# Performance work log

Hardware: AMD Instinct MI355X
Metric: run time of the kernel (lower is better)

## Reference

```python
import jax, jax.numpy as jnp
import numpy as np

D_MODEL = 1024
N_HEADS = 16
D_K = D_MODEL // N_HEADS
LN_EPS = 1e-5


def setup_inputs() -> dict:
    key = jax.random.key(0)
    ks = jax.random.split(key, 10)
    s = 1.0 / np.sqrt(D_MODEL)
    x = jax.random.normal(ks[0], (8, 1024, D_MODEL), dtype=jnp.float32)
    return {
        "x": x,
        "Wq": jax.random.uniform(ks[1], (D_MODEL, D_MODEL), jnp.float32, -s, s),
        "bq": jax.random.uniform(ks[2], (D_MODEL,), jnp.float32, -s, s),
        "Wk": jax.random.uniform(ks[3], (D_MODEL, D_MODEL), jnp.float32, -s, s),
        "bk": jax.random.uniform(ks[4], (D_MODEL,), jnp.float32, -s, s),
        "Wv": jax.random.uniform(ks[5], (D_MODEL, D_MODEL), jnp.float32, -s, s),
        "bv": jax.random.uniform(ks[6], (D_MODEL,), jnp.float32, -s, s),
        "Wo": jax.random.uniform(ks[7], (D_MODEL, D_MODEL), jnp.float32, -s, s),
        "bo": jax.random.uniform(ks[8], (D_MODEL,), jnp.float32, -s, s),
        "gamma": jnp.ones((D_MODEL,), jnp.float32),
        "beta": jnp.zeros((D_MODEL,), jnp.float32),
    }


def reference(x, Wq, bq, Wk, bk, Wv, bv, Wo, bo, gamma, beta):
    B, S, D = x.shape
    H, dk = N_HEADS, D_K
    # projections -> [B, H, S, dk]
    q = (x @ Wq.T + bq).reshape(B, S, H, dk).transpose(0, 2, 1, 3)
    k = (x @ Wk.T + bk).reshape(B, S, H, dk).transpose(0, 2, 1, 3)
    v = (x @ Wv.T + bv).reshape(B, S, H, dk).transpose(0, 2, 1, 3)
    scores = jnp.einsum('bhqd,bhkd->bhqk', q, k) / jnp.sqrt(jnp.float32(dk))
    attn = jax.nn.softmax(scores, axis=-1)  # dropout: eval mode (identity)
    ctx = jnp.einsum('bhqk,bhkd->bhqd', attn, v)
    ctx = ctx.transpose(0, 2, 1, 3).reshape(B, S, D)
    out = ctx @ Wo.T + bo
    h = out + x  # residual
    mu = jnp.mean(h, axis=-1, keepdims=True)
    var = jnp.mean((h - mu) ** 2, axis=-1, keepdims=True)
    y = (h - mu) * jax.lax.rsqrt(var + LN_EPS) * gamma + beta
    return y, attn
```

## Files before the change

### kernel.cpp

```cpp
#include <hip/hip_runtime.h>
#include <math.h>

#define D 1024
#define H 16
#define DK 64
#define SQ 1024
#define NB 8
#define NROW (NB*SQ)

typedef __attribute__((ext_vector_type(8))) short bf16x8;
typedef __attribute__((ext_vector_type(4))) float f32x4;

__device__ __forceinline__ ushort f2bf(float x){
    unsigned u = __builtin_bit_cast(unsigned, x);
    u += 0x7FFFu + ((u >> 16) & 1u);
    return (ushort)(u >> 16);
}
__device__ __forceinline__ float bf2f(ushort u){
    return __builtin_bit_cast(float, (unsigned)u << 16);
}

__device__ __forceinline__ f32x4 mfma16(bf16x8 a, bf16x8 b, f32x4 c){
    return __builtin_amdgcn_mfma_f32_16x16x32_bf16(a, b, c, 0, 0, 0);
}

__device__ __forceinline__ void gload16(const void* g, void* l){
    __builtin_amdgcn_global_load_lds(
        (const __attribute__((address_space(1))) unsigned int*)g,
        (__attribute__((address_space(3))) unsigned int*)l, 16, 0, 0);
}

__device__ __forceinline__ bf16x8 gld8(const ushort* p){
    return __builtin_bit_cast(bf16x8, *(const uint4*)p);
}

__global__ __launch_bounds__(256)
void cvt_all(const float* __restrict__ x,
             const float* __restrict__ Wq, const float* __restrict__ Wk,
             const float* __restrict__ Wv, const float* __restrict__ Wo,
             ushort* __restrict__ xb, ushort* __restrict__ wb_)
{
    const int bid = blockIdx.x;
    const float* s; ushort* d; size_t off;
    if (bid < 4096) { s = x; d = xb; off = (size_t)bid * 2048; }
    else {
        int r = bid - 4096;
        int wsel = r >> 9;
        if      (wsel == 0) s = Wq;
        else if (wsel == 1) s = Wk;
        else if (wsel == 2) s = Wv;
        else                s = Wo;
        d = wb_ + (size_t)wsel * 1048576;
        off = (size_t)(r & 511) * 2048;
    }
    size_t i = off + (size_t)threadIdx.x * 8;
    float4 a = *(const float4*)(s + i);
    float4 b = *(const float4*)(s + i + 4);
    ushort tmp[8] = {f2bf(a.x),f2bf(a.y),f2bf(a.z),f2bf(a.w),
                     f2bf(b.x),f2bf(b.y),f2bf(b.z),f2bf(b.w)};
    *(uint4*)(d + i) = *(uint4*)tmp;
}

__device__ __forceinline__ void stage_g(const ushort* __restrict__ g, int ldg,
                                        ushort* lds, int t)
{
#pragma unroll
    for (int i = 0; i < 2; ++i){
        int c = i*256 + t;
        int row = c >> 2, sc = c & 3;
        int gch = sc ^ (row & 3);
        gload16(g + (size_t)row*ldg + gch*8, lds + c*8);
    }
}
__device__ __forceinline__ bf16x8 gfrag(const ushort* lds, int row, int kc)
{
    uint4 v = ((const uint4*)lds)[row*4 + (kc ^ (row & 3))];
    return __builtin_bit_cast(bf16x8, v);
}

__global__ __launch_bounds__(256)
void gemm_qkv(const ushort* __restrict__ A, const ushort* __restrict__ Wp,
              const float* __restrict__ bq, const float* __restrict__ bk,
              const float* __restrict__ bv,
              ushort* __restrict__ Qb, ushort* __restrict__ Kb,
              ushort* __restrict__ Vtb)
{
    __shared__ ushort As[4096];
    __shared__ ushort Bs[4096];
    const int t = threadIdx.x, lane = t & 63, w = t >> 6;
    const int wr = w >> 1, wc = w & 1, lr = lane & 15, kg = lane >> 4;
    const int bx = blockIdx.x % 24, by = blockIdx.x / 24;
    const int i0 = by * 128, j0 = bx * 128;
    const int section = bx >> 3;
    const ushort* Ab = A  + (size_t)i0 * 1024;
    const ushort* Wb = Wp + (size_t)j0 * 1024;
    const float* bias = (section == 0) ? bq : (section == 1) ? bk : bv;
    ushort* outp      = (section == 0) ? Qb : (section == 1) ? Kb : Vtb;

    f32x4 acc[4][4];
#pragma unroll
    for (int m = 0; m < 4; ++m)
#pragma unroll
        for (int n = 0; n < 4; ++n) acc[m][n] = (f32x4){0.f,0.f,0.f,0.f};

    for (int k0 = 0; k0 < 1024; k0 += 32){
        __syncthreads();
        stage_g(Ab + k0, 1024, As, t);
        stage_g(Wb + k0, 1024, Bs, t);
        __syncthreads();
        bf16x8 af[4], bfr[4];
#pragma unroll
        for (int m = 0; m < 4; ++m) af[m]  = gfrag(As, wr*64 + m*16 + lr, kg);
#pragma unroll
        for (int n = 0; n < 4; ++n) bfr[n] = gfrag(Bs, wc*64 + n*16 + lr, kg);
#pragma unroll
        for (int m = 0; m < 4; ++m)
#pragma unroll
            for (int n = 0; n < 4; ++n)
                acc[m][n] = mfma16(af[m], bfr[n], acc[m][n]);
    }

#pragma unroll
    for (int m = 0; m < 4; ++m){
        int rt = i0 + wr*64 + m*16 + kg*4;
#pragma unroll
        for (int n = 0; n < 4; ++n){
            int jc = ((j0 + wc*64 + n*16 + lr) & 1023);
            float bj = bias[jc];
            int hh = jc >> 6, dd = jc & 63;
#pragma unroll
            for (int j = 0; j < 4; ++j){
                int i = rt + j;
                int b = i >> 10, s = i & 1023;
                float v = acc[m][n][j] + bj;
                size_t idx = (section < 2)
                    ? ((((size_t)b*H + hh)*SQ + s)*DK + dd)
                    : ((((size_t)b*H + hh)*DK + dd)*SQ + s);
                outp[idx] = f2bf(v);
            }
        }
    }
}

__global__ __launch_bounds__(256)
void gemm_o(const ushort* __restrict__ A, const ushort* __restrict__ W,
            const float* __restrict__ bias, const float* __restrict__ resid,
            float* __restrict__ out)
{
    __shared__ ushort As[4096];
    __shared__ ushort Bs[4096];
    const int t = threadIdx.x, lane = t & 63, w = t >> 6;
    const int wr = w >> 1, wc = w & 1, lr = lane & 15, kg = lane >> 4;
    const int i0 = blockIdx.y * 128, j0 = blockIdx.x * 128;
    const ushort* Ab = A + (size_t)i0 * 1024;
    const ushort* Wb = W + (size_t)j0 * 1024;

    f32x4 acc[4][4];
#pragma unroll
    for (int m = 0; m < 4; ++m)
#pragma unroll
        for (int n = 0; n < 4; ++n) acc[m][n] = (f32x4){0.f,0.f,0.f,0.f};

    for (int k0 = 0; k0 < 1024; k0 += 32){
        __syncthreads();
        stage_g(Ab + k0, 1024, As, t);
        stage_g(Wb + k0, 1024, Bs, t);
        __syncthreads();
        bf16x8 af[4], bfr[4];
#pragma unroll
        for (int m = 0; m < 4; ++m) af[m]  = gfrag(As, wr*64 + m*16 + lr, kg);
#pragma unroll
        for (int n = 0; n < 4; ++n) bfr[n] = gfrag(Bs, wc*64 + n*16 + lr, kg);
#pragma unroll
        for (int m = 0; m < 4; ++m)
#pragma unroll
            for (int n = 0; n < 4; ++n)
                acc[m][n] = mfma16(af[m], bfr[n], acc[m][n]);
    }

#pragma unroll
    for (int m = 0; m < 4; ++m){
        int rt = i0 + wr*64 + m*16 + kg*4;
#pragma unroll
        for (int n = 0; n < 4; ++n){
            int ct = j0 + wc*64 + n*16 + lr;
            float bj = bias[ct];
#pragma unroll
            for (int j = 0; j < 4; ++j){
                int i = rt + j;
                out[(size_t)i*1024 + ct] = acc[m][n][j] + bj + resid[(size_t)i*1024 + ct];
            }
        }
    }
}

__device__ __forceinline__ void stage64x64(const ushort* __restrict__ g, int ldg,
                                           ushort* lds, int t)
{
#pragma unroll
    for (int i = 0; i < 2; ++i){
        int c = i*256 + t;
        int row = c >> 3, sc = c & 7;
        int gch = sc ^ (row & 7);
        gload16(g + (size_t)row*ldg + gch*8, lds + c*8);
    }
}
__device__ __forceinline__ bf16x8 frag_ld(const ushort* lds, int row, int chunk)
{
    uint4 v = ((const uint4*)lds)[row*8 + (chunk ^ (row & 7))];
    return __builtin_bit_cast(bf16x8, v);
}

__global__ __launch_bounds__(256)
void attn_v6(const ushort* __restrict__ Q, const ushort* __restrict__ K,
             const ushort* __restrict__ Vt, float* __restrict__ attn_out,
             ushort* __restrict__ ctx)
{
    __shared__ ushort KV[2][8192];
    __shared__ ushort Ps[4][1024];

    const int t    = threadIdx.x;
    const int lane = t & 63;
    const int w    = t >> 6;
    const int lr   = lane & 15, kg = lane >> 4;
    const int bid  = blockIdx.x;
    const int qt   = bid >> 7, bh = bid & 127;
    const int b    = bh >> 4, hh = bh & 15;
    const size_t base = (size_t)bh * SQ * DK;

    bf16x8 qf[2];
    {
        const ushort* qrow = Q + base + (size_t)(qt*64 + w*16 + lr) * DK + kg*8;
        qf[0] = gld8(qrow);
        qf[1] = gld8(qrow + 32);
    }

    const float CEXP = 0.18033688011112042f;

    float lsum[4] = {0.f, 0.f, 0.f, 0.f};
    stage64x64(K + base, DK, KV[0], t);
    for (int kt = 0; kt < 16; ++kt) {
        const int cur = kt & 1;
        __syncthreads();
        if (kt < 15)
            stage64x64(K + base + (size_t)(kt+1)*64*DK, DK, KV[cur^1], t);
        const ushort* Ks = KV[cur];
#pragma unroll
        for (int n = 0; n < 4; ++n) {
            f32x4 z = {0.f,0.f,0.f,0.f};
            z = mfma16(qf[0], frag_ld(Ks, n*16+lr, kg),   z);
            z = mfma16(qf[1], frag_ld(Ks, n*16+lr, 4+kg), z);
#pragma unroll
            for (int r = 0; r < 4; ++r)
                lsum[r] += exp2f(z[r] * CEXP);
        }
    }
    float invl[4];
#pragma unroll
    for (int r = 0; r < 4; ++r) {
        float s = lsum[r];
#pragma unroll
        for (int msk = 1; msk < 16; msk <<= 1) s += __shfl_xor(s, msk, 64);
        invl[r] = 1.0f / s;
    }

    f32x4 acc_o[4];
#pragma unroll
    for (int n = 0; n < 4; ++n) acc_o[n] = (f32x4){0.f,0.f,0.f,0.f};

    float* ap0 = attn_out + ((size_t)bh*SQ + (size_t)qt*64 + w*16)*SQ;
    ushort* pw = &Ps[w][0];

    stage64x64(K  + base, DK, KV[0],        t);
    stage64x64(Vt + base, SQ, KV[0] + 4096, t);

    for (int kt = 0; kt < 16; ++kt) {
        const int cur = kt & 1;
        __syncthreads();
        if (kt < 15) {
            stage64x64(K  + base + (size_t)(kt+1)*64*DK, DK, KV[cur^1],        t);
            stage64x64(Vt + base + (size_t)(kt+1)*64,    SQ, KV[cur^1] + 4096, t);
        }
        const ushort* Ks = KV[cur];
        const ushort* Vs = KV[cur] + 4096;

        f32x4 sc[4];
#pragma unroll
        for (int n = 0; n < 4; ++n) {
            f32x4 z = {0.f,0.f,0.f,0.f};
            z = mfma16(qf[0], frag_ld(Ks, n*16+lr, kg),   z);
            z = mfma16(qf[1], frag_ld(Ks, n*16+lr, 4+kg), z);
            sc[n] = z;
        }
#pragma unroll
        for (int n = 0; n < 4; ++n) {
#pragma unroll
            for (int r = 0; r < 4; ++r) {
                float p = exp2f(sc[n][r] * CEXP) * invl[r];
                int row = kg*4 + r, col = n*16 + lr;
                pw[row*64 + ((col>>3) ^ (row&7))*8 + (col&7)] = f2bf(p);
            }
        }
        bf16x8 a0 = frag_ld(pw, lr, kg);
        bf16x8 a1 = frag_ld(pw, lr, 4+kg);
#pragma unroll
        for (int n = 0; n < 4; ++n) {
            acc_o[n] = mfma16(a0, frag_ld(Vs, n*16+lr, kg),   acc_o[n]);
            acc_o[n] = mfma16(a1, frag_ld(Vs, n*16+lr, 4+kg), acc_o[n]);
        }
#pragma unroll
        for (int rr = 0; rr < 4; ++rr) {
            int row = kg*4 + rr;
            int cidx = row*64 + ((lr>>1) ^ (row&7))*8 + (lr&1)*4;
            uint2 pk = *(const uint2*)(pw + cidx);
            float4 o;
            o.x = bf2f((ushort)(pk.x & 0xFFFF));
            o.y = bf2f((ushort)(pk.x >> 16));
            o.z = bf2f((ushort)(pk.y & 0xFFFF));
            o.w = bf2f((ushort)(pk.y >> 16));
            *(float4*)(ap0 + (size_t)row*SQ + kt*64 + lr*4) = o;
        }
    }

    ushort* cp = ctx + ((size_t)b*SQ + (size_t)qt*64 + w*16)*D + hh*DK;
#pragma unroll
    for (int n = 0; n < 4; ++n)
#pragma unroll
        for (int r = 0; r < 4; ++r)
            cp[(size_t)(kg*4+r)*D + n*16 + lr] = f2bf(acc_o[n][r]);
}

__global__ __launch_bounds__(256)
void ln_k(const float* __restrict__ hbuf, const float* __restrict__ gamma,
          const float* __restrict__ beta, float* __restrict__ y)
{
    const int row = blockIdx.x, t = threadIdx.x;
    float4 v = ((const float4*)(hbuf + (size_t)row * D))[t];
    float s  = v.x + v.y + v.z + v.w;
    float sq = v.x*v.x + v.y*v.y + v.z*v.z + v.w*v.w;
#pragma unroll
    for (int o = 32; o >= 1; o >>= 1) {
        s  += __shfl_down(s, o, 64);
        sq += __shfl_down(sq, o, 64);
    }
    __shared__ float rs_[4], rq_[4], mu_s, rstd_s;
    int wid = t >> 6;
    if ((t & 63) == 0) { rs_[wid] = s; rq_[wid] = sq; }
    __syncthreads();
    if (t == 0) {
        float S  = rs_[0]+rs_[1]+rs_[2]+rs_[3];
        float Q2 = rq_[0]+rq_[1]+rq_[2]+rq_[3];
        float mu  = S * (1.0f/1024.0f);
        float var = Q2 * (1.0f/1024.0f) - mu*mu;
        mu_s = mu; rstd_s = rsqrtf(var + 1e-5f);
    }
    __syncthreads();
    float mu = mu_s, rstd = rstd_s;
    float4 g = ((const float4*)gamma)[t];
    float4 be = ((const float4*)beta)[t];
    float4 o;
    o.x = (v.x-mu)*rstd*g.x + be.x;
    o.y = (v.y-mu)*rstd*g.y + be.y;
    o.z = (v.z-mu)*rstd*g.z + be.z;
    o.w = (v.w-mu)*rstd*g.w + be.w;
    ((float4*)(y + (size_t)row * D))[t] = o;
}

extern "C" void kernel_launch(void* const* d_in, const int* in_sizes, int n_in,
                              void* d_out, int out_size, void* d_ws, size_t ws_size,
                              hipStream_t stream)
{
    const float* x     = (const float*)d_in[0];
    const float* Wq    = (const float*)d_in[1];
    const float* bq    = (const float*)d_in[2];
    const float* Wk    = (const float*)d_in[3];
    const float* bk    = (const float*)d_in[4];
    const float* Wv    = (const float*)d_in[5];
    const float* bv    = (const float*)d_in[6];
    const float* Wo    = (const float*)d_in[7];
    const float* bo    = (const float*)d_in[8];
    const float* gamma = (const float*)d_in[9];
    const float* beta  = (const float*)d_in[10];

    float* y    = (float*)d_out;
    float* attn = (float*)d_out + (size_t)NROW * D;

    const size_t SZ  = (size_t)NROW * D;
    const size_t WSZ = (size_t)D * D;
    ushort* ws   = (ushort*)d_ws;
    ushort* xb   = ws;
    ushort* Wpk  = xb  + SZ;
    ushort* Wob  = Wpk + 3*WSZ;
    ushort* Qb   = Wob + WSZ;
    ushort* Kb   = Qb  + SZ;
    ushort* Vtb  = Kb  + SZ;
    ushort* Cb   = Vtb + SZ;
    float*  Hb   = (float*)(Cb + SZ);

    cvt_all<<<6144, 256, 0, stream>>>(x, Wq, Wk, Wv, Wo, xb, Wpk);

    gemm_qkv<<<1536, 256, 0, stream>>>(xb, Wpk, bq, bk, bv, Qb, Kb, Vtb);

    attn_v6<<<2048, 256, 0, stream>>>(Qb, Kb, Vtb, attn, Cb);

    gemm_o<<<dim3(8, 64), 256, 0, stream>>>(Cb, Wob, bo, x, Hb);

    ln_k<<<NROW, 256, 0, stream>>>(Hb, gamma, beta, y);
}
```

Measured before the change: 336.2 us.

## Process 128 query rows per attention block with 512 threads and MFMA priority

The attention kernel now launches half as many blocks, each with 8 waves covering 128 query rows instead of 64, so every staged K/V tile in LDS serves twice as many queries. The staging helper is rewritten so each of the 512 threads loads one 16-byte chunk. The per-wave P scratch buffer grows to 8 slots. s_setprio calls raise wave priority around the MFMA sections so matrix work is favoured over other waves' memory work. The larger block may lower occupancy and scheduling flexibility on a kernel that is largely bound by writing the attention matrix.

```diff
diff --git a/kernel.cpp b/kernel.cpp
--- a/kernel.cpp
+++ b/kernel.cpp
@@ -194,16 +194,12 @@
     }
 }
 
-__device__ __forceinline__ void stage64x64(const ushort* __restrict__ g, int ldg,
-                                           ushort* lds, int t)
-{
-#pragma unroll
-    for (int i = 0; i < 2; ++i){
-        int c = i*256 + t;
-        int row = c >> 3, sc = c & 7;
-        int gch = sc ^ (row & 7);
-        gload16(g + (size_t)row*ldg + gch*8, lds + c*8);
-    }
+__device__ __forceinline__ void stage64x64_512(const ushort* __restrict__ g, int ldg,
+                                               ushort* lds, int t)
+{
+    int row = t >> 3, sc = t & 7;
+    int gch = sc ^ (row & 7);
+    gload16(g + (size_t)row*ldg + gch*8, lds + t*8);
 }
 __device__ __forceinline__ bf16x8 frag_ld(const ushort* lds, int row, int chunk)
 {
@@ -211,13 +207,13 @@
     return __builtin_bit_cast(bf16x8, v);
 }
 
-__global__ __launch_bounds__(256)
-void attn_v6(const ushort* __restrict__ Q, const ushort* __restrict__ K,
+__global__ __launch_bounds__(512)
+void attn_v8(const ushort* __restrict__ Q, const ushort* __restrict__ K,
              const ushort* __restrict__ Vt, float* __restrict__ attn_out,
              ushort* __restrict__ ctx)
 {
     __shared__ ushort KV[2][8192];
-    __shared__ ushort Ps[4][1024];
+    __shared__ ushort Ps[8][1024];
 
     const int t    = threadIdx.x;
     const int lane = t & 63;
@@ -230,7 +226,7 @@
 
     bf16x8 qf[2];
     {
-        const ushort* qrow = Q + base + (size_t)(qt*64 + w*16 + lr) * DK + kg*8;
+        const ushort* qrow = Q + base + (size_t)(qt*128 + w*16 + lr) * DK + kg*8;
         qf[0] = gld8(qrow);
         qf[1] = gld8(qrow + 32);
     }
@@ -238,13 +234,14 @@
     const float CEXP = 0.18033688011112042f;
 
     float lsum[4] = {0.f, 0.f, 0.f, 0.f};
-    stage64x64(K + base, DK, KV[0], t);
+    stage64x64_512(K + base, DK, KV[0], t);
     for (int kt = 0; kt < 16; ++kt) {
         const int cur = kt & 1;
         __syncthreads();
         if (kt < 15)
-            stage64x64(K + base + (size_t)(kt+1)*64*DK, DK, KV[cur^1], t);
+            stage64x64_512(K + base + (size_t)(kt+1)*64*DK, DK, KV[cur^1], t);
         const ushort* Ks = KV[cur];
+        __builtin_amdgcn_s_setprio(1);
 #pragma unroll
         for (int n = 0; n < 4; ++n) {
             f32x4 z = {0.f,0.f,0.f,0.f};
@@ -254,6 +251,7 @@
             for (int r = 0; r < 4; ++r)
                 lsum[r] += exp2f(z[r] * CEXP);
         }
+        __builtin_amdgcn_s_setprio(0);
     }
     float invl[4];
 #pragma unroll
@@ -268,23 +266,24 @@
 #pragma unroll
     for (int n = 0; n < 4; ++n) acc_o[n] = (f32x4){0.f,0.f,0.f,0.f};
 
-    float* ap0 = attn_out + ((size_t)bh*SQ + (size_t)qt*64 + w*16)*SQ;
+    float* ap0 = attn_out + ((size_t)bh*SQ + (size_t)qt*128 + w*16)*SQ;
     ushort* pw = &Ps[w][0];
 
-    stage64x64(K  + base, DK, KV[0],        t);
-    stage64x64(Vt + base, SQ, KV[0] + 4096, t);
+    stage64x64_512(K  + base, DK, KV[0],        t);
+    stage64x64_512(Vt + base, SQ, KV[0] + 4096, t);
 
     for (int kt = 0; kt < 16; ++kt) {
         const int cur = kt & 1;
         __syncthreads();
         if (kt < 15) {
-            stage64x64(K  + base + (size_t)(kt+1)*64*DK, DK, KV[cur^1],        t);
-            stage64x64(Vt + base + (size_t)(kt+1)*64,    SQ, KV[cur^1] + 4096, t);
+            stage64x64_512(K  + base + (size_t)(kt+1)*64*DK, DK, KV[cur^1],        t);
+            stage64x64_512(Vt + base + (size_t)(kt+1)*64,    SQ, KV[cur^1] + 4096, t);
         }
         const ushort* Ks = KV[cur];
         const ushort* Vs = KV[cur] + 4096;
 
         f32x4 sc[4];
+        __builtin_amdgcn_s_setprio(1);
 #pragma unroll
         for (int n = 0; n < 4; ++n) {
             f32x4 z = {0.f,0.f,0.f,0.f};
@@ -292,6 +291,7 @@
             z = mfma16(qf[1], frag_ld(Ks, n*16+lr, 4+kg), z);
             sc[n] = z;
         }
+        __builtin_amdgcn_s_setprio(0);
 #pragma unroll
         for (int n = 0; n < 4; ++n) {
 #pragma unroll
@@ -303,11 +303,13 @@
         }
         bf16x8 a0 = frag_ld(pw, lr, kg);
         bf16x8 a1 = frag_ld(pw, lr, 4+kg);
+        __builtin_amdgcn_s_setprio(1);
 #pragma unroll
         for (int n = 0; n < 4; ++n) {
             acc_o[n] = mfma16(a0, frag_ld(Vs, n*16+lr, kg),   acc_o[n]);
             acc_o[n] = mfma16(a1, frag_ld(Vs, n*16+lr, 4+kg), acc_o[n]);
         }
+        __builtin_amdgcn_s_setprio(0);
 #pragma unroll
         for (int rr = 0; rr < 4; ++rr) {
             int row = kg*4 + rr;
@@ -322,7 +324,7 @@
         }
     }
 
-    ushort* cp = ctx + ((size_t)b*SQ + (size_t)qt*64 + w*16)*D + hh*DK;
+    ushort* cp = ctx + ((size_t)b*SQ + (size_t)qt*128 + w*16)*D + hh*DK;
 #pragma unroll
     for (int n = 0; n < 4; ++n)
 #pragma unroll
@@ -401,7 +403,7 @@
 
     gemm_qkv<<<1536, 256, 0, stream>>>(xb, Wpk, bq, bk, bv, Qb, Kb, Vtb);
 
-    attn_v6<<<2048, 256, 0, stream>>>(Qb, Kb, Vtb, attn, Cb);
+    attn_v8<<<1024, 512, 0, stream>>>(Qb, Kb, Vtb, attn, Cb);
 
     gemm_o<<<dim3(8, 64), 256, 0, stream>>>(Cb, Wob, bo, x, Hb);
 
```

After: 349.0 us. 1.04x slower.

## Split attention into unnormalized ctx pass and separate attn-matrix write kernel

Applied to the files above, without the earlier changes.

The fused attention kernel used to run two passes over K: one for row sums and one for probabilities, ctx and the attn matrix. It now computes ctx from unnormalized exponentials, accumulates the row sums in the same loop, scales ctx at the end and saves the inverse sums to a buffer. A new second kernel recomputes QK^T and writes the normalized fp32 attn matrix. This takes V loads and the bf16 round-trip out of the attn-write path but adds a kernel launch. The attn values are no longer bf16-rounded, and the written attn is in a strided per-lane pattern rather than float4 stores.

```diff
diff --git a/kernel.cpp b/kernel.cpp
--- a/kernel.cpp
+++ b/kernel.cpp
@@ -15,9 +15,6 @@
     unsigned u = __builtin_bit_cast(unsigned, x);
     u += 0x7FFFu + ((u >> 16) & 1u);
     return (ushort)(u >> 16);
-}
-__device__ __forceinline__ float bf2f(ushort u){
-    return __builtin_bit_cast(float, (unsigned)u << 16);
 }
 
 __device__ __forceinline__ f32x4 mfma16(bf16x8 a, bf16x8 b, f32x4 c){
@@ -212,9 +209,9 @@
 }
 
 __global__ __launch_bounds__(256)
-void attn_v6(const ushort* __restrict__ Q, const ushort* __restrict__ K,
-             const ushort* __restrict__ Vt, float* __restrict__ attn_out,
-             ushort* __restrict__ ctx)
+void attn_ctx(const ushort* __restrict__ Q, const ushort* __restrict__ K,
+              const ushort* __restrict__ Vt, float* __restrict__ invb,
+              ushort* __restrict__ ctx)
 {
     __shared__ ushort KV[2][8192];
     __shared__ ushort Ps[4][1024];
@@ -238,37 +235,10 @@
     const float CEXP = 0.18033688011112042f;
 
     float lsum[4] = {0.f, 0.f, 0.f, 0.f};
-    stage64x64(K + base, DK, KV[0], t);
-    for (int kt = 0; kt < 16; ++kt) {
-        const int cur = kt & 1;
-        __syncthreads();
-        if (kt < 15)
-            stage64x64(K + base + (size_t)(kt+1)*64*DK, DK, KV[cur^1], t);
-        const ushort* Ks = KV[cur];
-#pragma unroll
-        for (int n = 0; n < 4; ++n) {
-            f32x4 z = {0.f,0.f,0.f,0.f};
-            z = mfma16(qf[0], frag_ld(Ks, n*16+lr, kg),   z);
-            z = mfma16(qf[1], frag_ld(Ks, n*16+lr, 4+kg), z);
-#pragma unroll
-            for (int r = 0; r < 4; ++r)
-                lsum[r] += exp2f(z[r] * CEXP);
-        }
-    }
-    float invl[4];
-#pragma unroll
-    for (int r = 0; r < 4; ++r) {
-        float s = lsum[r];
-#pragma unroll
-        for (int msk = 1; msk < 16; msk <<= 1) s += __shfl_xor(s, msk, 64);
-        invl[r] = 1.0f / s;
-    }
-
     f32x4 acc_o[4];
 #pragma unroll
     for (int n = 0; n < 4; ++n) acc_o[n] = (f32x4){0.f,0.f,0.f,0.f};
 
-    float* ap0 = attn_out + ((size_t)bh*SQ + (size_t)qt*64 + w*16)*SQ;
     ushort* pw = &Ps[w][0];
 
     stage64x64(K  + base, DK, KV[0],        t);
@@ -294,11 +264,13 @@
         }
 #pragma unroll
         for (int n = 0; n < 4; ++n) {
+            const int col = n*16 + lr;
 #pragma unroll
             for (int r = 0; r < 4; ++r) {
-                float p = exp2f(sc[n][r] * CEXP) * invl[r];
-                int row = kg*4 + r, col = n*16 + lr;
-                pw[row*64 + ((col>>3) ^ (row&7))*8 + (col&7)] = f2bf(p);
+                float e = exp2f(sc[n][r] * CEXP);
+                lsum[r] += e;
+                int row = kg*4 + r;
+                pw[row*64 + ((col>>3) ^ (row&7))*8 + (col&7)] = f2bf(e);
             }
         }
         bf16x8 a0 = frag_ld(pw, lr, kg);
@@ -308,18 +280,21 @@
             acc_o[n] = mfma16(a0, frag_ld(Vs, n*16+lr, kg),   acc_o[n]);
             acc_o[n] = mfma16(a1, frag_ld(Vs, n*16+lr, 4+kg), acc_o[n]);
         }
-#pragma unroll
-        for (int rr = 0; rr < 4; ++rr) {
-            int row = kg*4 + rr;
-            int cidx = row*64 + ((lr>>1) ^ (row&7))*8 + (lr&1)*4;
-            uint2 pk = *(const uint2*)(pw + cidx);
-            float4 o;
-            o.x = bf2f((ushort)(pk.x & 0xFFFF));
-            o.y = bf2f((ushort)(pk.x >> 16));
-            o.z = bf2f((ushort)(pk.y & 0xFFFF));
-            o.w = bf2f((ushort)(pk.y >> 16));
-            *(float4*)(ap0 + (size_t)row*SQ + kt*64 + lr*4) = o;
-        }
+    }
+
+    float invl[4];
+#pragma unroll
+    for (int r = 0; r < 4; ++r) {
+        float s = lsum[r];
+#pragma unroll
+        for (int msk = 1; msk < 16; msk <<= 1) s += __shfl_xor(s, msk, 64);
+        invl[r] = 1.0f / s;
+    }
+
+    if (lr == 0) {
+        float* ivp = invb + (size_t)bh*SQ + qt*64 + w*16 + kg*4;
+#pragma unroll
+        for (int r = 0; r < 4; ++r) ivp[r] = invl[r];
     }
 
     ushort* cp = ctx + ((size_t)b*SQ + (size_t)qt*64 + w*16)*D + hh*DK;
@@ -327,7 +302,65 @@
     for (int n = 0; n < 4; ++n)
 #pragma unroll
         for (int r = 0; r < 4; ++r)
-            cp[(size_t)(kg*4+r)*D + n*16 + lr] = f2bf(acc_o[n][r]);
+            cp[(size_t)(kg*4+r)*D + n*16 + lr] = f2bf(acc_o[n][r] * invl[r]);
+}
+
+__global__ __launch_bounds__(256)
+void attn_write(const ushort* __restrict__ Q, const ushort* __restrict__ K,
+                const float* __restrict__ invb, float* __restrict__ attn_out)
+{
+    __shared__ ushort Kb2[2][4096];
+
+    const int t    = threadIdx.x;
+    const int lane = t & 63;
+    const int w    = t >> 6;
+    const int lr   = lane & 15, kg = lane >> 4;
+    const int bid  = blockIdx.x;
+    const int qt   = bid >> 7, bh = bid & 127;
+    const size_t base = (size_t)bh * SQ * DK;
+
+    bf16x8 qf[2];
+    {
+        const ushort* qrow = Q + base + (size_t)(qt*64 + w*16 + lr) * DK + kg*8;
+        qf[0] = gld8(qrow);
+        qf[1] = gld8(qrow + 32);
+    }
+    float invl[4];
+    {
+        const float* ivp = invb + (size_t)bh*SQ + qt*64 + w*16 + kg*4;
+#pragma unroll
+        for (int r = 0; r < 4; ++r) invl[r] = ivp[r];
+    }
+
+    const float CEXP = 0.18033688011112042f;
+    float* ap0 = attn_out + ((size_t)bh*SQ + (size_t)qt*64 + w*16)*SQ;
+
+    stage64x64(K + base, DK, Kb2[0], t);
+
+    for (int kt = 0; kt < 16; ++kt) {
+        const int cur = kt & 1;
+        __syncthreads();
+        if (kt < 15)
+            stage64x64(K + base + (size_t)(kt+1)*64*DK, DK, Kb2[cur^1], t);
+        const ushort* Ks = Kb2[cur];
+
+        f32x4 sc[4];
+#pragma unroll
+        for (int n = 0; n < 4; ++n) {
+            f32x4 z = {0.f,0.f,0.f,0.f};
+            z = mfma16(qf[0], frag_ld(Ks, n*16+lr, kg),   z);
+            z = mfma16(qf[1], frag_ld(Ks, n*16+lr, 4+kg), z);
+            sc[n] = z;
+        }
+#pragma unroll
+        for (int n = 0; n < 4; ++n) {
+#pragma unroll
+            for (int r = 0; r < 4; ++r) {
+                float p = exp2f(sc[n][r] * CEXP) * invl[r];
+                ap0[(size_t)(kg*4+r)*SQ + kt*64 + n*16 + lr] = p;
+            }
+        }
+    }
 }
 
 __global__ __launch_bounds__(256)
@@ -396,12 +429,15 @@
     ushort* Vtb  = Kb  + SZ;
     ushort* Cb   = Vtb + SZ;
     float*  Hb   = (float*)(Cb + SZ);
+    float*  invb = Hb + SZ;
 
     cvt_all<<<6144, 256, 0, stream>>>(x, Wq, Wk, Wv, Wo, xb, Wpk);
 
     gemm_qkv<<<1536, 256, 0, stream>>>(xb, Wpk, bq, bk, bv, Qb, Kb, Vtb);
 
-    attn_v6<<<2048, 256, 0, stream>>>(Qb, Kb, Vtb, attn, Cb);
+    attn_ctx<<<2048, 256, 0, stream>>>(Qb, Kb, Vtb, invb, Cb);
+
+    attn_write<<<2048, 256, 0, stream>>>(Qb, Kb, invb, attn);
 
     gemm_o<<<dim3(8, 64), 256, 0, stream>>>(Cb, Wob, bo, x, Hb);
 
```

New measurement: 387.2 us. +15.2%, slower.
